# Performance work log

Measured on AMD Instinct MI355X. Metric: run time of the kernel, lower is better.

The kernel has to match this reference:

```python
import jax, jax.numpy as jnp
import numpy as np

N_NODES = 100000
N_EDGES = 1600000
D_IN = 128
D_HID = 128
N_CLASSES = 40


def _glorot(key, fan_in, fan_out):
    lim = np.sqrt(6.0 / (fan_in + fan_out)).astype(np.float32)
    return jax.random.uniform(key, (fan_in, fan_out), jnp.float32, -lim, lim)


def setup_inputs() -> dict:
    key = jax.random.key(0)
    ks = jax.random.split(key, 10)
    x = jax.random.normal(ks[0], (N_NODES, D_IN), jnp.float32)
    edge_index = jax.random.randint(ks[1], (2, N_EDGES), 0, N_NODES, jnp.int64)
    return {
        "x": x,
        "edge_index": edge_index,
        # layer 1: lin_l (neighbor, with bias), lin_r (root, no bias)
        "W1l": _glorot(ks[2], D_IN, D_HID),
        "b1": jnp.zeros((D_HID,), jnp.float32),
        "W1r": _glorot(ks[3], D_IN, D_HID),
        # layer 2
        "W2l": _glorot(ks[4], D_HID, D_HID),
        "b2": jnp.zeros((D_HID,), jnp.float32),
        "W2r": _glorot(ks[5], D_HID, D_HID),
        # layer 3
        "W3l": _glorot(ks[6], D_HID, N_CLASSES),
        "b3": jnp.zeros((N_CLASSES,), jnp.float32),
        "W3r": _glorot(ks[7], D_HID, N_CLASSES),
    }


def _sage_conv(x, src, dst, deg_inv, Wl, bl, Wr):
    # mean aggregation of source-node features onto destination nodes
    msgs = x[src]                                            # [E, d] gather
    agg = jax.ops.segment_sum(msgs, dst, num_segments=N_NODES)  # [N, d]
    agg = agg * deg_inv[:, None]                             # mean
    return agg @ Wl + bl + x @ Wr


def reference(x, edge_index, W1l, b1, W1r, W2l, b2, W2r, W3l, b3, W3r):
    src, dst = edge_index[0], edge_index[1]
    deg = jax.ops.segment_sum(jnp.ones((N_EDGES,), x.dtype), dst,
                              num_segments=N_NODES)
    deg_inv = 1.0 / jnp.maximum(deg, 1.0)
    h = _sage_conv(x, src, dst, deg_inv, W1l, b1, W1r)
    h = jax.nn.relu(h)  # dropout is identity in eval mode
    h = _sage_conv(h, src, dst, deg_inv, W2l, b2, W2r)
    h = jax.nn.relu(h)
    h = _sage_conv(h, src, dst, deg_inv, W3l, b3, W3r)
    return jax.nn.log_softmax(h, axis=1)
```

## Files before the change

kernel.cpp:

```cpp
#include <hip/hip_runtime.h>
#include <math.h>

#define D 128
#define NCLS 40
#define NBLK_P1 256

typedef unsigned int u32;
typedef __attribute__((ext_vector_type(8))) short short8;
typedef __attribute__((ext_vector_type(4))) float f32x4;

__device__ inline float bflo(u32 u){ return __uint_as_float(u << 16); }
__device__ inline float bfhi(u32 u){ return __uint_as_float(u & 0xffff0000u); }
__device__ inline u32 pack2bf(float a, float b){
  u32 ua = __float_as_uint(a), ub = __float_as_uint(b);
  ua += 0x7fffu + ((ua >> 16) & 1u);
  ub += 0x7fffu + ((ub >> 16) & 1u);
  return (ua >> 16) | (ub & 0xffff0000u);
}
__device__ inline unsigned short pack1bf(float a){
  u32 ua = __float_as_uint(a);
  ua += 0x7fffu + ((ua >> 16) & 1u);
  return (unsigned short)(ua >> 16);
}

__global__ __launch_bounds__(256) void prep_k(
    const float4* __restrict__ x4, uint2* __restrict__ xb, int n4,
    const float* __restrict__ W1l, const float* __restrict__ W1r, u32* __restrict__ Wt1,
    const float* __restrict__ W2l, const float* __restrict__ W2r, u32* __restrict__ Wt2,
    const float* __restrict__ W3l, const float* __restrict__ W3r,
    u32* __restrict__ Wt3b, float* __restrict__ bias3b, const float* __restrict__ b3,
    int* __restrict__ deg, int N, int nbX)
{
  const int b = blockIdx.x;
  const int tid = threadIdx.x;
  if (b < nbX){
    int i = b * 256 + tid;
    if (i < n4){
      float4 v = x4[i];
      xb[i] = make_uint2(pack2bf(v.x, v.y), pack2bf(v.z, v.w));
    }
  } else if (b < nbX + 128){
    const bool first = (b < nbX + 64);
    const float* Wl = first ? W1l : W2l;
    const float* Wr = first ? W1r : W2r;
    u32* Wt = first ? Wt1 : Wt2;
    int i = ((b - nbX) & 63) * 256 + tid;
    int nn = i >> 7, kp = i & 127;
    int k = kp * 2;
    float a, c;
    if (k < 128){ a = Wl[(size_t)k * 128 + nn]; c = Wl[(size_t)(k + 1) * 128 + nn]; }
    else        { a = Wr[(size_t)(k - 128) * 128 + nn]; c = Wr[(size_t)(k - 127) * 128 + nn]; }
    Wt[(size_t)nn * 128 + kp] = pack2bf(a, c);
  } else if (b < nbX + 160){
    int i = (b - nbX - 128) * 256 + tid;
    if (i < 128 * 64){
      int nn = i >> 6, kp = i & 63;
      int k = kp * 2;
      float a = 0.f, c = 0.f;
      if (nn < NCLS){
        a = W3l[(size_t)k * NCLS + nn]; c = W3l[(size_t)(k + 1) * NCLS + nn];
      } else if (nn >= 64 && nn < 64 + NCLS){
        int cc = nn - 64;
        a = W3r[(size_t)k * NCLS + cc]; c = W3r[(size_t)(k + 1) * NCLS + cc];
      }
      Wt3b[(size_t)nn * 64 + kp] = pack2bf(a, c);
    }
    if (b == nbX + 128 && tid < 128)
      bias3b[tid] = (tid >= 64 && tid < 64 + NCLS) ? b3[tid - 64] : 0.f;
  } else {
    int i = (b - nbX - 160) * 256 + tid;
    if (i < N) deg[i] = 0;
  }
}


__global__ __launch_bounds__(256) void part_hist_k(
    const int* __restrict__ dst, int* __restrict__ deg,
    int* __restrict__ gcnt, int E, int nbuk)
{
  __shared__ int cnt[1024];
  const int tid = threadIdx.x;
  for (int i = tid; i < nbuk; i += 256) cnt[i] = 0;
  __syncthreads();
  const int per = (E + NBLK_P1 - 1) / NBLK_P1;
  const int e0 = blockIdx.x * per;
  const int e1 = min(e0 + per, E);
  for (int i = e0 + tid; i < e1; i += 256){
    int d = dst[i];
    atomicAdd(&deg[d], 1);
    atomicAdd(&cnt[d >> 7], 1);
  }
  __syncthreads();
  for (int i = tid; i < nbuk; i += 256)
    gcnt[(size_t)blockIdx.x * nbuk + i] = cnt[i];
}

__global__ void scan_excl_k(const int* __restrict__ in, int* __restrict__ out,
                            int* __restrict__ bsum, int n){
  __shared__ int sm[1024];
  int tid = threadIdx.x;
  int i = blockIdx.x * blockDim.x + tid;
  int v = (i < n) ? in[i] : 0;
  sm[tid] = v; __syncthreads();
  int acc = v;
  for (int off = 1; off < (int)blockDim.x; off <<= 1){
    int t = (tid >= off) ? sm[tid - off] : 0;
    __syncthreads();
    acc += t; sm[tid] = acc;
    __syncthreads();
  }
  if (i < n) out[i] = acc - v;
  if (bsum && tid == (int)blockDim.x - 1) bsum[blockIdx.x] = acc;
}

__global__ void finalize_k(int* __restrict__ csr_off, const int* __restrict__ bsum_s,
                           const int* __restrict__ deg, float* __restrict__ deg_inv,
                           int n, int E){
  int i = blockIdx.x * blockDim.x + threadIdx.x;
  if (i < n){
    csr_off[i] += bsum_s[i >> 10];
    deg_inv[i] = 1.0f / fmaxf((float)deg[i], 1.0f);
  }
  if (i == 0) csr_off[n] = E;
}

__global__ __launch_bounds__(256) void part_scan_k(
    const int* __restrict__ csr_off, const int* __restrict__ gcnt,
    int* __restrict__ goff, int N, int nbuk)
{
  int j = blockIdx.x * 256 + threadIdx.x;
  if (j >= nbuk) return;
  int acc = csr_off[min(j << 7, N)];
  for (int i = 0; i < NBLK_P1; i++){
    int t = gcnt[(size_t)i * nbuk + j];
    goff[(size_t)i * nbuk + j] = acc;
    acc += t;
  }
}

__global__ __launch_bounds__(256) void part_fill_k(
    const int* __restrict__ src, const int* __restrict__ dst,
    const int* __restrict__ goff, u32* __restrict__ staging,
    int E, int nbuk)
{
  __shared__ int boff[1024];
  __shared__ int cur[1024];
  const int tid = threadIdx.x;
  for (int i = tid; i < nbuk; i += 256){
    boff[i] = goff[(size_t)blockIdx.x * nbuk + i];
    cur[i] = 0;
  }
  __syncthreads();
  const int per = (E + NBLK_P1 - 1) / NBLK_P1;
  const int e0 = blockIdx.x * per;
  const int e1 = min(e0 + per, E);
  for (int i = e0 + tid; i < e1; i += 256){
    int d = dst[i];
    int s = src[i];
    int b = d >> 7;
    int p = atomicAdd(&cur[b], 1);
    staging[boff[b] + p] = ((u32)s << 7) | (u32)(d & 127);
  }
}

__global__ __launch_bounds__(256) void bucket_csr_k(
    const u32* __restrict__ staging, const int* __restrict__ coff,
    int* __restrict__ csr_src, int N)
{
  __shared__ int lpos[128];
  __shared__ int lbase[129];
  const int node0 = blockIdx.x << 7;
  const int tid = threadIdx.x;
  if (tid < 128) lpos[tid] = 0;
  if (tid < 129) lbase[tid] = coff[min(node0 + tid, N)];
  __syncthreads();
  const int lo = lbase[0], hi = lbase[128];
  for (int i = lo + tid; i < hi; i += 256){
    u32 v = staging[i];
    int dloc = (int)(v & 127u);
    int p = atomicAdd(&lpos[dloc], 1);
    csr_src[lbase[dloc] + p] = (int)(v >> 7);
  }
}

__device__ inline void add8(float* acc, uint4 v){
  acc[0] += bflo(v.x); acc[1] += bfhi(v.x);
  acc[2] += bflo(v.y); acc[3] += bfhi(v.y);
  acc[4] += bflo(v.z); acc[5] += bfhi(v.z);
  acc[6] += bflo(v.w); acc[7] += bfhi(v.w);
}

__global__ __launch_bounds__(256) void aggregate_k(
    const u32* __restrict__ feat, const int* __restrict__ coff,
    const int* __restrict__ csr_src, const float* __restrict__ deg_inv,
    u32* __restrict__ agg, int n)
{
  const int g = threadIdx.x >> 4;
  const int lane = threadIdx.x & 15;
  const int node = blockIdx.x * 16 + g;
  if (node >= n) return;
  const int lo = coff[node], hi = coff[node + 1];
  const uint4* __restrict__ f4 = (const uint4*)feat;
  float acc[8] = {0.f,0.f,0.f,0.f,0.f,0.f,0.f,0.f};
  int e = lo;
  for (; e + 3 < hi; e += 4){
    int s0 = csr_src[e], s1 = csr_src[e + 1];
    int s2 = csr_src[e + 2], s3 = csr_src[e + 3];
    uint4 v0 = f4[(size_t)s0 * 16 + lane];
    uint4 v1 = f4[(size_t)s1 * 16 + lane];
    uint4 v2 = f4[(size_t)s2 * 16 + lane];
    uint4 v3 = f4[(size_t)s3 * 16 + lane];
    add8(acc, v0); add8(acc, v1); add8(acc, v2); add8(acc, v3);
  }
  for (; e < hi; ++e){
    uint4 v0 = f4[(size_t)csr_src[e] * 16 + lane];
    add8(acc, v0);
  }
  const float di = deg_inv[node];
  uint4 o;
  o.x = pack2bf(acc[0] * di, acc[1] * di);
  o.y = pack2bf(acc[2] * di, acc[3] * di);
  o.z = pack2bf(acc[4] * di, acc[5] * di);
  o.w = pack2bf(acc[6] * di, acc[7] * di);
  ((uint4*)agg)[(size_t)node * 16 + lane] = o;
}

__global__ __launch_bounds__(256) void gemm_mfma_k(
    const u32* __restrict__ A1, const u32* __restrict__ A2,
    const u32* __restrict__ Wt, const float* __restrict__ bias,
    u32* __restrict__ out, int n)
{
  __shared__ u32 As_u[128 * 20];
  __shared__ u32 Bs_u[128 * 20];
  const int tid = threadIdx.x;
  const int row0 = blockIdx.x * 128;
  const int l = tid & 63, w = tid >> 6;
  const int lm = l & 15, lq = l >> 4;

  f32x4 acc[2][8];
  #pragma unroll
  for (int mi = 0; mi < 2; mi++)
    #pragma unroll
    for (int ni = 0; ni < 8; ni++) acc[mi][ni] = (f32x4){0.f, 0.f, 0.f, 0.f};

  for (int kt = 0; kt < 8; ++kt){
    const u32* Ap = (kt < 4) ? A1 : A2;
    const int ko = (kt & 3) * 16;
    #pragma unroll
    for (int i = 0; i < 2; i++){
      int chunk = tid + 256 * i;
      int row = chunk >> 2, q = chunk & 3;
      uint4 av = make_uint4(0, 0, 0, 0);
      int gr = row0 + row;
      if (gr < n) av = *(const uint4*)(Ap + (size_t)gr * 64 + ko + q * 4);
      *(uint4*)&As_u[row * 20 + q * 4] = av;
      uint4 bv = *(const uint4*)(Wt + (size_t)row * 128 + kt * 16 + q * 4);
      *(uint4*)&Bs_u[row * 20 + q * 4] = bv;
    }
    __syncthreads();
    short8 af0 = *(const short8*)&As_u[(w * 32 + lm) * 20 + lq * 4];
    short8 af1 = *(const short8*)&As_u[(w * 32 + 16 + lm) * 20 + lq * 4];
    #pragma unroll
    for (int ni = 0; ni < 8; ni++){
      short8 bf = *(const short8*)&Bs_u[(ni * 16 + lm) * 20 + lq * 4];
      acc[0][ni] = __builtin_amdgcn_mfma_f32_16x16x32_bf16(af0, bf, acc[0][ni], 0, 0, 0);
      acc[1][ni] = __builtin_amdgcn_mfma_f32_16x16x32_bf16(af1, bf, acc[1][ni], 0, 0, 0);
    }
    __syncthreads();
  }

  float bb[8];
  #pragma unroll
  for (int ni = 0; ni < 8; ni++) bb[ni] = bias[ni * 16 + lm];
  unsigned short* outp = (unsigned short*)out;
  #pragma unroll
  for (int mi = 0; mi < 2; mi++){
    #pragma unroll
    for (int r = 0; r < 4; r++){
      int row = row0 + w * 32 + mi * 16 + lq * 4 + r;
      if (row < n){
        #pragma unroll
        for (int ni = 0; ni < 8; ni++){
          float v = fmaxf(acc[mi][ni][r] + bb[ni], 0.f);
          outp[(size_t)row * 128 + ni * 16 + lm] = pack1bf(v);
        }
      }
    }
  }
}

__global__ __launch_bounds__(256) void gemm3_mfma_k(
    const u32* __restrict__ A, const u32* __restrict__ Wt3b,
    const float* __restrict__ bias, u32* __restrict__ out, int n)
{
  __shared__ u32 As_u[128 * 20];
  __shared__ u32 Bs_u[128 * 20];
  const int tid = threadIdx.x;
  const int row0 = blockIdx.x * 128;
  const int l = tid & 63, w = tid >> 6;
  const int lm = l & 15, lq = l >> 4;

  f32x4 acc[2][8];
  #pragma unroll
  for (int mi = 0; mi < 2; mi++)
    #pragma unroll
    for (int ni = 0; ni < 8; ni++) acc[mi][ni] = (f32x4){0.f, 0.f, 0.f, 0.f};

  for (int kt = 0; kt < 4; ++kt){
    #pragma unroll
    for (int i = 0; i < 2; i++){
      int chunk = tid + 256 * i;
      int row = chunk >> 2, q = chunk & 3;
      uint4 av = make_uint4(0, 0, 0, 0);
      int gr = row0 + row;
      if (gr < n) av = *(const uint4*)(A + (size_t)gr * 64 + kt * 16 + q * 4);
      *(uint4*)&As_u[row * 20 + q * 4] = av;
      uint4 bv = *(const uint4*)(Wt3b + (size_t)row * 64 + kt * 16 + q * 4);
      *(uint4*)&Bs_u[row * 20 + q * 4] = bv;
    }
    __syncthreads();
    short8 af0 = *(const short8*)&As_u[(w * 32 + lm) * 20 + lq * 4];
    short8 af1 = *(const short8*)&As_u[(w * 32 + 16 + lm) * 20 + lq * 4];
    #pragma unroll
    for (int ni = 0; ni < 8; ni++){
      short8 bf = *(const short8*)&Bs_u[(ni * 16 + lm) * 20 + lq * 4];
      acc[0][ni] = __builtin_amdgcn_mfma_f32_16x16x32_bf16(af0, bf, acc[0][ni], 0, 0, 0);
      acc[1][ni] = __builtin_amdgcn_mfma_f32_16x16x32_bf16(af1, bf, acc[1][ni], 0, 0, 0);
    }
    __syncthreads();
  }

  float bb[8];
  #pragma unroll
  for (int ni = 0; ni < 8; ni++) bb[ni] = bias[ni * 16 + lm];
  unsigned short* outp = (unsigned short*)out;
  #pragma unroll
  for (int mi = 0; mi < 2; mi++){
    #pragma unroll
    for (int r = 0; r < 4; r++){
      int row = row0 + w * 32 + mi * 16 + lq * 4 + r;
      if (row < n){
        #pragma unroll
        for (int ni = 0; ni < 8; ni++){
          float v = acc[mi][ni][r] + bb[ni];
          outp[(size_t)row * 128 + ni * 16 + lm] = pack1bf(v);
        }
      }
    }
  }
}

__global__ __launch_bounds__(256) void agg_softmax_k(
    const u32* __restrict__ yz, const int* __restrict__ coff,
    const int* __restrict__ csr_src, const float* __restrict__ deg_inv,
    float* __restrict__ out, int n)
{
  const int g = threadIdx.x >> 3;
  const int lane = threadIdx.x & 7;
  const int node = blockIdx.x * 32 + g;
  if (node >= n) return;
  const int lo = coff[node], hi = coff[node + 1];
  const uint4* __restrict__ f4 = (const uint4*)yz;
  float acc[8] = {0.f,0.f,0.f,0.f,0.f,0.f,0.f,0.f};
  int e = lo;
  for (; e + 3 < hi; e += 4){
    int s0 = csr_src[e], s1 = csr_src[e + 1];
    int s2 = csr_src[e + 2], s3 = csr_src[e + 3];
    uint4 v0 = f4[(size_t)s0 * 16 + lane];
    uint4 v1 = f4[(size_t)s1 * 16 + lane];
    uint4 v2 = f4[(size_t)s2 * 16 + lane];
    uint4 v3 = f4[(size_t)s3 * 16 + lane];
    add8(acc, v0); add8(acc, v1); add8(acc, v2); add8(acc, v3);
  }
  for (; e < hi; ++e){
    uint4 v0 = f4[(size_t)csr_src[e] * 16 + lane];
    add8(acc, v0);
  }
  const float di = deg_inv[node];
  uint4 zv = f4[(size_t)node * 16 + 8 + lane];
  float v[8];
  v[0] = acc[0] * di + bflo(zv.x); v[1] = acc[1] * di + bfhi(zv.x);
  v[2] = acc[2] * di + bflo(zv.y); v[3] = acc[3] * di + bfhi(zv.y);
  v[4] = acc[4] * di + bflo(zv.z); v[5] = acc[5] * di + bfhi(zv.z);
  v[6] = acc[6] * di + bflo(zv.w); v[7] = acc[7] * di + bfhi(zv.w);
  const bool valid = (lane < 5);
  float m = -INFINITY;
  if (valid){
    #pragma unroll
    for (int j = 0; j < 8; j++) m = fmaxf(m, v[j]);
  }
  #pragma unroll
  for (int off = 1; off < 8; off <<= 1) m = fmaxf(m, __shfl_xor(m, off, 64));
  float s = 0.f;
  if (valid){
    #pragma unroll
    for (int j = 0; j < 8; j++) s += __expf(v[j] - m);
  }
  #pragma unroll
  for (int off = 1; off < 8; off <<= 1) s += __shfl_xor(s, off, 64);
  const float ls = m + logf(s);
  if (valid){
    float* op = out + (size_t)node * NCLS + lane * 8;
    *(float4*)op     = make_float4(v[0]-ls, v[1]-ls, v[2]-ls, v[3]-ls);
    *(float4*)(op+4) = make_float4(v[4]-ls, v[5]-ls, v[6]-ls, v[7]-ls);
  }
}


extern "C" void kernel_launch(void* const* d_in, const int* in_sizes, int n_in,
                              void* d_out, int out_size, void* d_ws, size_t ws_size,
                              hipStream_t stream) {
  const float* x   = (const float*)d_in[0];
  const int*   ei  = (const int*)d_in[1];
  const float* W1l = (const float*)d_in[2];
  const float* b1  = (const float*)d_in[3];
  const float* W1r = (const float*)d_in[4];
  const float* W2l = (const float*)d_in[5];
  const float* b2  = (const float*)d_in[6];
  const float* W2r = (const float*)d_in[7];
  const float* W3l = (const float*)d_in[8];
  const float* b3  = (const float*)d_in[9];
  const float* W3r = (const float*)d_in[10];

  const int N = in_sizes[0] / D;
  const int E = in_sizes[1] / 2;
  const int* src = ei;
  const int* dst = ei + E;
  const int nbuk = (N + 127) >> 7;

  char* ws = (char*)d_ws;
  auto alloc = [&](size_t bytes) -> void* {
    void* p = (void*)ws;
    ws += (bytes + 255) & ~(size_t)255;
    return p;
  };
  int*   deg_i    = (int*)  alloc((size_t)N * 4);
  int*   csr_off  = (int*)  alloc((size_t)(N + 1) * 4);
  int*   bsum     = (int*)  alloc(1024);
  int*   bsum_s   = (int*)  alloc(1024);
  float* deg_inv  = (float*)alloc((size_t)N * 4);
  int*   csr_src  = (int*)  alloc((size_t)E * 4);
  u32*   staging  = (u32*)  alloc((size_t)E * 4);
  int*   gcnt     = (int*)  alloc((size_t)NBLK_P1 * nbuk * 4);
  int*   goff     = (int*)  alloc((size_t)NBLK_P1 * nbuk * 4);
  u32*   xb       = (u32*)  alloc((size_t)N * D * 2);
  u32*   agg      = (u32*)  alloc((size_t)N * D * 2);
  u32*   hbuf     = (u32*)  alloc((size_t)N * D * 2);
  u32*   yz       = (u32*)  alloc((size_t)N * D * 2);
  u32*   Wt1      = (u32*)  alloc((size_t)128 * 128 * 4);
  u32*   Wt2      = (u32*)  alloc((size_t)128 * 128 * 4);
  u32*   Wt3b     = (u32*)  alloc((size_t)128 * 64 * 4);
  float* bias3b   = (float*)alloc((size_t)128 * 4);

  const int n4 = N * D / 4;
  const int nbX = (n4 + 255) / 256;
  const int nbZ = (N + 255) / 256;
  prep_k<<<nbX + 160 + nbZ, 256, 0, stream>>>(
      (const float4*)x, (uint2*)xb, n4,
      W1l, W1r, Wt1, W2l, W2r, Wt2,
      W3l, W3r, Wt3b, bias3b, b3,
      deg_i, N, nbX);

  part_hist_k<<<NBLK_P1, 256, 0, stream>>>(dst, deg_i, gcnt, E, nbuk);
  const int NB = (N + 1023) / 1024;
  scan_excl_k<<<NB, 1024, 0, stream>>>(deg_i, csr_off, bsum, N);
  scan_excl_k<<<1, 128, 0, stream>>>(bsum, bsum_s, nullptr, NB);
  finalize_k<<<(N + 255) / 256, 256, 0, stream>>>(csr_off, bsum_s, deg_i, deg_inv, N, E);
  part_scan_k<<<(nbuk + 255) / 256, 256, 0, stream>>>(csr_off, gcnt, goff, N, nbuk);
  part_fill_k<<<NBLK_P1, 256, 0, stream>>>(src, dst, goff, staging, E, nbuk);
  bucket_csr_k<<<nbuk, 256, 0, stream>>>(staging, csr_off, csr_src, N);

  const int gblocks = (N + 127) / 128;
  const int ablocks = (N + 15) / 16;
  aggregate_k<<<ablocks, 256, 0, stream>>>(xb, csr_off, csr_src, deg_inv, agg, N);
  gemm_mfma_k<<<gblocks, 256, 0, stream>>>(agg, xb, Wt1, b1, hbuf, N);
  aggregate_k<<<ablocks, 256, 0, stream>>>(hbuf, csr_off, csr_src, deg_inv, agg, N);
  gemm_mfma_k<<<gblocks, 256, 0, stream>>>(agg, hbuf, Wt2, b2, hbuf, N);
  gemm3_mfma_k<<<gblocks, 256, 0, stream>>>(hbuf, Wt3b, bias3b, yz, N);
  agg_softmax_k<<<(N + 31) / 32, 256, 0, stream>>>(yz, csr_off, csr_src, deg_inv,
                                                   (float*)d_out, N);
}
```

Before: 459.7 us.

## Derive node degrees and CSR offsets per bucket instead of a global degree scan

Removes the global per-node degree histogram, which did 1.6M global atomics, along with the two-level exclusive scan and the finalize kernel. Bucket totals are now scanned in a single 1024-thread block. Each bucket_csr block counts local degrees in shared memory, scans them, and writes csr_off and deg_inv itself. This cuts three launches and the global atomic traffic, at the cost of a serial single-block bucket scan and an extra pass over the staging data.

```diff
diff --git a/kernel.cpp b/kernel.cpp
--- a/kernel.cpp
+++ b/kernel.cpp
@@ -29,7 +29,7 @@
     const float* __restrict__ W2l, const float* __restrict__ W2r, u32* __restrict__ Wt2,
     const float* __restrict__ W3l, const float* __restrict__ W3r,
     u32* __restrict__ Wt3b, float* __restrict__ bias3b, const float* __restrict__ b3,
-    int* __restrict__ deg, int N, int nbX)
+    int nbX)
 {
   const int b = blockIdx.x;
   const int tid = threadIdx.x;
@@ -51,7 +51,7 @@
     if (k < 128){ a = Wl[(size_t)k * 128 + nn]; c = Wl[(size_t)(k + 1) * 128 + nn]; }
     else        { a = Wr[(size_t)(k - 128) * 128 + nn]; c = Wr[(size_t)(k - 127) * 128 + nn]; }
     Wt[(size_t)nn * 128 + kp] = pack2bf(a, c);
-  } else if (b < nbX + 160){
+  } else {
     int i = (b - nbX - 128) * 256 + tid;
     if (i < 128 * 64){
       int nn = i >> 6, kp = i & 63;
@@ -67,16 +67,12 @@
     }
     if (b == nbX + 128 && tid < 128)
       bias3b[tid] = (tid >= 64 && tid < 64 + NCLS) ? b3[tid - 64] : 0.f;
-  } else {
-    int i = (b - nbX - 160) * 256 + tid;
-    if (i < N) deg[i] = 0;
   }
 }
 
 
 __global__ __launch_bounds__(256) void part_hist_k(
-    const int* __restrict__ dst, int* __restrict__ deg,
-    int* __restrict__ gcnt, int E, int nbuk)
+    const int* __restrict__ dst, int* __restrict__ gcnt, int E, int nbuk)
 {
   __shared__ int cnt[1024];
   const int tid = threadIdx.x;
@@ -85,56 +81,40 @@
   const int per = (E + NBLK_P1 - 1) / NBLK_P1;
   const int e0 = blockIdx.x * per;
   const int e1 = min(e0 + per, E);
-  for (int i = e0 + tid; i < e1; i += 256){
-    int d = dst[i];
-    atomicAdd(&deg[d], 1);
-    atomicAdd(&cnt[d >> 7], 1);
-  }
+  for (int i = e0 + tid; i < e1; i += 256)
+    atomicAdd(&cnt[dst[i] >> 7], 1);
   __syncthreads();
   for (int i = tid; i < nbuk; i += 256)
     gcnt[(size_t)blockIdx.x * nbuk + i] = cnt[i];
 }
 
-__global__ void scan_excl_k(const int* __restrict__ in, int* __restrict__ out,
-                            int* __restrict__ bsum, int n){
+__global__ __launch_bounds__(1024) void part_scan_k(
+    const int* __restrict__ gcnt, int* __restrict__ goff,
+    int* __restrict__ bbase, int nbuk)
+{
   __shared__ int sm[1024];
-  int tid = threadIdx.x;
-  int i = blockIdx.x * blockDim.x + tid;
-  int v = (i < n) ? in[i] : 0;
-  sm[tid] = v; __syncthreads();
-  int acc = v;
-  for (int off = 1; off < (int)blockDim.x; off <<= 1){
-    int t = (tid >= off) ? sm[tid - off] : 0;
-    __syncthreads();
-    acc += t; sm[tid] = acc;
-    __syncthreads();
-  }
-  if (i < n) out[i] = acc - v;
-  if (bsum && tid == (int)blockDim.x - 1) bsum[blockIdx.x] = acc;
-}
-
-__global__ void finalize_k(int* __restrict__ csr_off, const int* __restrict__ bsum_s,
-                           const int* __restrict__ deg, float* __restrict__ deg_inv,
-                           int n, int E){
-  int i = blockIdx.x * blockDim.x + threadIdx.x;
-  if (i < n){
-    csr_off[i] += bsum_s[i >> 10];
-    deg_inv[i] = 1.0f / fmaxf((float)deg[i], 1.0f);
-  }
-  if (i == 0) csr_off[n] = E;
-}
-
-__global__ __launch_bounds__(256) void part_scan_k(
-    const int* __restrict__ csr_off, const int* __restrict__ gcnt,
-    int* __restrict__ goff, int N, int nbuk)
-{
-  int j = blockIdx.x * 256 + threadIdx.x;
-  if (j >= nbuk) return;
-  int acc = csr_off[min(j << 7, N)];
-  for (int i = 0; i < NBLK_P1; i++){
-    int t = gcnt[(size_t)i * nbuk + j];
-    goff[(size_t)i * nbuk + j] = acc;
-    acc += t;
+  const int j = threadIdx.x;
+  int btot = 0;
+  if (j < nbuk)
+    for (int i = 0; i < NBLK_P1; i++) btot += gcnt[(size_t)i * nbuk + j];
+  sm[j] = btot;
+  __syncthreads();
+  int acc = btot;
+  for (int off = 1; off < 1024; off <<= 1){
+    int t = (j >= off) ? sm[j - off] : 0;
+    __syncthreads();
+    acc += t; sm[j] = acc;
+    __syncthreads();
+  }
+  const int base = acc - btot;
+  if (j < nbuk){
+    bbase[j] = base;
+    if (j == nbuk - 1) bbase[nbuk] = base + btot;
+    int run = base;
+    for (int i = 0; i < NBLK_P1; i++){
+      goff[(size_t)i * nbuk + j] = run;
+      run += gcnt[(size_t)i * nbuk + j];
+    }
   }
 }
 
@@ -164,17 +144,45 @@
 }
 
 __global__ __launch_bounds__(256) void bucket_csr_k(
-    const u32* __restrict__ staging, const int* __restrict__ coff,
+    const u32* __restrict__ staging, const int* __restrict__ bbase,
+    int* __restrict__ csr_off, float* __restrict__ deg_inv,
     int* __restrict__ csr_src, int N)
 {
+  __shared__ int ldeg[128];
+  __shared__ int sm[128];
+  __shared__ int lbase[128];
   __shared__ int lpos[128];
-  __shared__ int lbase[129];
-  const int node0 = blockIdx.x << 7;
-  const int tid = threadIdx.x;
-  if (tid < 128) lpos[tid] = 0;
-  if (tid < 129) lbase[tid] = coff[min(node0 + tid, N)];
-  __syncthreads();
-  const int lo = lbase[0], hi = lbase[128];
+  const int b = blockIdx.x;
+  const int node0 = b << 7;
+  const int tid = threadIdx.x;
+  if (tid < 128) ldeg[tid] = 0;
+  __syncthreads();
+  const int lo = bbase[b], hi = bbase[b + 1];
+  for (int i = lo + tid; i < hi; i += 256)
+    atomicAdd(&ldeg[staging[i] & 127u], 1);
+  __syncthreads();
+  if (tid < 128) sm[tid] = ldeg[tid];
+  __syncthreads();
+  for (int off = 1; off < 128; off <<= 1){
+    int t = (tid >= off && tid < 128) ? sm[tid - off] : 0;
+    __syncthreads();
+    if (tid < 128) sm[tid] += t;
+    __syncthreads();
+  }
+  if (tid < 128){
+    const int excl = sm[tid] - ldeg[tid];
+    lbase[tid] = lo + excl;
+    lpos[tid] = 0;
+    const int node = node0 + tid;
+    if (node < N){
+      csr_off[node] = lo + excl;
+      deg_inv[node] = 1.0f / fmaxf((float)ldeg[tid], 1.0f);
+    } else if (node == N){
+      csr_off[N] = lo + excl;
+    }
+  }
+  if (tid == 0 && b == (int)gridDim.x - 1) csr_off[N] = hi;
+  __syncthreads();
   for (int i = lo + tid; i < hi; i += 256){
     u32 v = staging[i];
     int dloc = (int)(v & 127u);
@@ -434,41 +442,33 @@
     ws += (bytes + 255) & ~(size_t)255;
     return p;
   };
-  int*   deg_i    = (int*)  alloc((size_t)N * 4);
   int*   csr_off  = (int*)  alloc((size_t)(N + 1) * 4);
-  int*   bsum     = (int*)  alloc(1024);
-  int*   bsum_s   = (int*)  alloc(1024);
   float* deg_inv  = (float*)alloc((size_t)N * 4);
   int*   csr_src  = (int*)  alloc((size_t)E * 4);
   u32*   staging  = (u32*)  alloc((size_t)E * 4);
   int*   gcnt     = (int*)  alloc((size_t)NBLK_P1 * nbuk * 4);
   int*   goff     = (int*)  alloc((size_t)NBLK_P1 * nbuk * 4);
+  int*   bbase    = (int*)  alloc((size_t)(nbuk + 1) * 4);
   u32*   xb       = (u32*)  alloc((size_t)N * D * 2);
   u32*   agg      = (u32*)  alloc((size_t)N * D * 2);
   u32*   hbuf     = (u32*)  alloc((size_t)N * D * 2);
   u32*   yz       = (u32*)  alloc((size_t)N * D * 2);
   u32*   Wt1      = (u32*)  alloc((size_t)128 * 128 * 4);
   u32*   Wt2      = (u32*)  alloc((size_t)128 * 128 * 4);
-  u32*   Wt3b     = (u32*)  alloc((size_t)128 * 64 * 4);
+  u32*   Wt3b    = (u32*)  alloc((size_t)128 * 64 * 4);
   float* bias3b   = (float*)alloc((size_t)128 * 4);
 
   const int n4 = N * D / 4;
   const int nbX = (n4 + 255) / 256;
-  const int nbZ = (N + 255) / 256;
-  prep_k<<<nbX + 160 + nbZ, 256, 0, stream>>>(
+  prep_k<<<nbX + 160, 256, 0, stream>>>(
       (const float4*)x, (uint2*)xb, n4,
       W1l, W1r, Wt1, W2l, W2r, Wt2,
-      W3l, W3r, Wt3b, bias3b, b3,
-      deg_i, N, nbX);
-
-  part_hist_k<<<NBLK_P1, 256, 0, stream>>>(dst, deg_i, gcnt, E, nbuk);
-  const int NB = (N + 1023) / 1024;
-  scan_excl_k<<<NB, 1024, 0, stream>>>(deg_i, csr_off, bsum, N);
-  scan_excl_k<<<1, 128, 0, stream>>>(bsum, bsum_s, nullptr, NB);
-  finalize_k<<<(N + 255) / 256, 256, 0, stream>>>(csr_off, bsum_s, deg_i, deg_inv, N, E);
-  part_scan_k<<<(nbuk + 255) / 256, 256, 0, stream>>>(csr_off, gcnt, goff, N, nbuk);
+      W3l, W3r, Wt3b, bias3b, b3, nbX);
+
+  part_hist_k<<<NBLK_P1, 256, 0, stream>>>(dst, gcnt, E, nbuk);
+  part_scan_k<<<1, 1024, 0, stream>>>(gcnt, goff, bbase, nbuk);
   part_fill_k<<<NBLK_P1, 256, 0, stream>>>(src, dst, goff, staging, E, nbuk);
-  bucket_csr_k<<<nbuk, 256, 0, stream>>>(staging, csr_off, csr_src, N);
+  bucket_csr_k<<<nbuk, 256, 0, stream>>>(staging, bbase, csr_off, deg_inv, csr_src, N);
 
   const int gblocks = (N + 127) / 128;
   const int ablocks = (N + 15) / 16;
```

Measured after the change: 409.2 us. -11.0%, faster.
